# Performance work log

Measured on AMD Instinct MI355X. Metric: run time of the kernel, lower is better.

The kernel has to match this reference:

```python
import jax, jax.numpy as jnp
import numpy as np

B = 1024      # number of states
NP = 32       # SVGD particles per state
AD = 20       # act_dim
OD = 64       # obs_dim
H = 256       # critic hidden width
STEPS = 5     # num_svgd_steps
LR = 0.1      # svgd_lr (adaptive_lr disabled)
SP0 = 1.0     # svgd_sigma_p0
ALIM = 1.0    # act_limit


def _q(obs, X, w1, b1, w2, b2, w3, b3):
    h = jnp.concatenate([obs, X], axis=-1)
    h = jax.nn.relu(h @ w1 + b1)
    h = jax.nn.relu(h @ w2 + b2)
    return jnp.squeeze(h @ w3 + b3, -1)


def _rbf(X):
    # X: [B, NP, AD] -> K [B,NP,NP], diff [B,NP,NP,AD], gamma [B,1,1], K_grad [B,NP,NP,AD]
    diff = X[:, :, None, :] - X[:, None, :, :]
    dist_sq = jnp.sum(diff * diff, axis=-1)
    # adaptive bandwidth via median heuristic (adaptive_sig=True)
    med = jnp.median(dist_sq.reshape(dist_sq.shape[0], -1), axis=-1)
    sig_sq = med / (2.0 * jnp.log(NP + 1.0))
    gamma = (1.0 / (2.0 * sig_sq + 1e-8))[:, None, None]
    K = jnp.exp(-gamma * dist_sq)
    K_grad = -2.0 * gamma[..., None] * diff * K[..., None]  # d/dx_i K(x_i, x_j)
    return K, diff, gamma, K_grad


def setup_inputs():
    key = jax.random.key(0)
    ks = jax.random.split(key, 16)
    N = B * NP

    def lin(k, fi, fo):
        return (jax.random.normal(k, (fi, fo), jnp.float32) / np.sqrt(fi)).astype(jnp.float32)

    return {
        "obs": jax.random.normal(ks[0], (N, OD), jnp.float32),
        "a0": jax.random.normal(ks[1], (N, AD), jnp.float32) * np.sqrt(SP0),
        "q1_w1": lin(ks[2], OD + AD, H), "q1_b1": jnp.zeros((H,), jnp.float32),
        "q1_w2": lin(ks[3], H, H),       "q1_b2": jnp.zeros((H,), jnp.float32),
        "q1_w3": lin(ks[4], H, 1),       "q1_b3": jnp.zeros((1,), jnp.float32),
        "q2_w1": lin(ks[5], OD + AD, H), "q2_b1": jnp.zeros((H,), jnp.float32),
        "q2_w2": lin(ks[6], H, H),       "q2_b2": jnp.zeros((H,), jnp.float32),
        "q2_w3": lin(ks[7], H, 1),       "q2_b3": jnp.zeros((1,), jnp.float32),
    }


def reference(obs, a0, q1_w1, q1_b1, q1_w2, q1_b2, q1_w3, q1_b3,
              q2_w1, q2_b1, q2_w2, q2_b2, q2_w3, q2_b3):
    eye = jnp.eye(NP, dtype=a0.dtype)

    def q_min_sum(Xf):
        q1 = _q(obs, Xf, q1_w1, q1_b1, q1_w2, q1_b2, q1_w3, q1_b3)
        q2 = _q(obs, Xf, q2_w1, q2_b1, q2_w2, q2_b2, q2_w3, q2_b3)
        return jnp.sum(jnp.minimum(q1, q2))

    score_fn = jax.grad(q_min_sum)  # autograd score function

    def step(carry, _):
        a, logp = carry
        score = score_fn(a).reshape(-1, NP, AD)                 # [B,NP,AD]
        X = a.reshape(-1, NP, AD)
        K, diff, gamma, Kg = _rbf(X)
        phi = (jnp.einsum('bij,bjd->bid', K, score) + Kg.sum(axis=1)) / NP
        # log-prob correction terms (with_logprob=True)
        term1 = jnp.mean(jnp.sum(Kg * score[:, None, :, :], axis=-1), axis=2)     # [B,NP]
        inner = jnp.sum(jnp.transpose(Kg, (0, 2, 1, 3)) * diff, axis=-1) \
                - AD * (K - eye)
        term2 = -2.0 * gamma[:, :, 0] * jnp.mean(inner, axis=1)                   # [B,NP]
        logp = logp - LR * (term1 + term2)
        a = a + LR * phi.reshape(a.shape)                        # svgd_optim
        return (a, logp), None

    logp0 = jnp.zeros((B, NP), a0.dtype)
    (a, logp_svgd), _ = jax.lax.scan(step, (a0, logp0), None, length=STEPS)

    a_sq = ALIM * jnp.tanh(a)                                    # [B*NP, AD]
    logp_normal = (-AD * 0.5 * jnp.log(2.0 * jnp.pi * SP0)
                   - 0.5 / SP0 * jnp.sum(a0 * a0, axis=-1)).reshape(-1, NP)
    logp_tanh = -jnp.sum(2.0 * (jnp.log(2.0) - a - jax.nn.softplus(-2.0 * a)),
                         axis=-1).reshape(-1, NP)
    logp_a = jnp.mean(logp_normal + logp_svgd + logp_tanh, axis=-1)  # [B]
    return a_sq, logp_a
```

## Files before the change

kernel.cpp:

```cpp
#include <hip/hip_runtime.h>
#include <math.h>

#define NPART 32
#define ADIM  20
#define ODIM  64
#define HID   256
#define NSTEPS 5
#define LRC   0.1f
#define NBLK  512

typedef short bf8 __attribute__((ext_vector_type(8)));
typedef float f4  __attribute__((ext_vector_type(4)));

#define OW1T(n) ((n)*24576)
#define OW2T(n) (49152 + (n)*65536)
#define OW2C(n) (180224 + (n)*65536)
#define OW1X(n) (311296 + (n)*8192)
#define OW3B(n) (327680 + (n)*256)
#define WS_ELEMS 328192

__device__ __forceinline__ short f2bf(float x) {
    unsigned u = __float_as_uint(x);
    u += 0x7FFFu + ((u >> 16) & 1u);
    return (short)(u >> 16);
}

#define MFMA(a,b,c) __builtin_amdgcn_mfma_f32_16x16x32_bf16((a),(b),(c),0,0,0)

__global__ void prep_weights(const float* __restrict__ w1a, const float* __restrict__ w2a,
                             const float* __restrict__ w3a, const float* __restrict__ w1b,
                             const float* __restrict__ w2b, const float* __restrict__ w3b,
                             unsigned short* __restrict__ ws)
{
    int idx = blockIdx.x * 256 + threadIdx.x;
    if (idx >= WS_ELEMS) return;
    float val;
    if (idx < 49152) {
        int net = idx / 24576, rem = idx % 24576;
        int n = rem / 96, k = rem % 96;
        const float* w1 = net ? w1b : w1a;
        val = (k < 84) ? w1[k*256 + n] : 0.f;
    } else if (idx < 180224) {
        int t2 = idx - 49152; int net = t2 / 65536, rem = t2 % 65536;
        int n = rem / 256, k = rem % 256;
        const float* w2 = net ? w2b : w2a;
        val = w2[k*256 + n];
    } else if (idx < 311296) {
        int t2 = idx - 180224; int net = t2 / 65536, rem = t2 % 65536;
        const float* w2 = net ? w2b : w2a;
        val = w2[rem];
    } else if (idx < 327680) {
        int t2 = idx - 311296; int net = t2 / 8192, rem = t2 % 8192;
        int d = rem / 256, n = rem % 256;
        const float* w1 = net ? w1b : w1a;
        val = (d < 20) ? w1[(64 + d)*256 + n] : 0.f;
    } else {
        int t2 = idx - 327680; int net = t2 / 256, k = t2 % 256;
        const float* w3 = net ? w3b : w3a;
        val = w3[k];
    }
    ws[idx] = (unsigned short)f2bf(val);
}

__global__ void __launch_bounds__(512, 4)
svgd_main(const float* __restrict__ obs,  const float* __restrict__ a0g,
          const float* __restrict__ b1a,  const float* __restrict__ b2a, const float* __restrict__ b3a,
          const float* __restrict__ b1b,  const float* __restrict__ b2b, const float* __restrict__ b3b,
          const float* __restrict__ w3af, const float* __restrict__ w3bf,
          const unsigned short* __restrict__ ws, float* __restrict__ out)
{
    __shared__ __align__(16) short A0s[64*96];
    __shared__ __align__(16) short hbuf[64*264];
    __shared__ unsigned maskS[2][2][64][8];
    __shared__ float Xm[64*20];
    __shared__ float scoreS[64*21];
    __shared__ float phis[64*20];
    __shared__ float qpart[2][8][64];
    __shared__ int   winsS[64];
    __shared__ float logps[64];
    __shared__ unsigned short lutI[496], lutJ[496];
    __shared__ float med2[4];
    __shared__ float qvS[64];

    const int t = threadIdx.x, b = blockIdx.x;
    const int lane = t & 63, wv = t >> 6;
    const int q = lane >> 4, mp = lane & 15;
    const int nb = wv * 32;

    for (int p = t; p < 64*ODIM; p += 512) {
        int i = p >> 6, d = p & 63;
        A0s[i*96 + d] = f2bf(obs[(b*64 + i)*ODIM + d]);
    }
    for (int p = t; p < 64*ADIM; p += 512) {
        int i = p / 20, d = p - i*20;
        float v = a0g[(b*64 + i)*20 + d];
        Xm[p] = v;
        A0s[i*96 + 64 + d] = f2bf(v);
    }
    for (int p = t; p < 64*12; p += 512) { int i = p/12, d = p - i*12; A0s[i*96 + 84 + d] = 0; }
    if (t < 496) {
        int i_ = 0, rem = t;
        while (rem >= 31 - i_) { rem -= 31 - i_; ++i_; }
        lutI[t] = (unsigned short)i_; lutJ[t] = (unsigned short)(i_ + 1 + rem);
    }
    if (t < 64) logps[t] = 0.f;
    __syncthreads();

    for (int step = 0; step < NSTEPS; ++step) {
        { unsigned* mz = &maskS[0][0][0][0];
          for (int p = t; p < 2*2*64*8; p += 512) mz[p] = 0u; }
        __syncthreads();

        for (int net = 0; net < 2; ++net) {
            const unsigned short* w1t = ws + OW1T(net);
            const unsigned short* w2t = ws + OW2T(net);
            const float* b1p = net ? b1b : b1a;
            const float* b2p = net ? b2b : b2a;
            const float* w3p = net ? w3bf : w3af;

            f4 acc[4][2];
            #pragma unroll
            for (int h = 0; h < 4; ++h) { acc[h][0] = (f4){0,0,0,0}; acc[h][1] = (f4){0,0,0,0}; }
            {
                const unsigned short* bp0 = w1t + (size_t)(nb +      mp)*96 + q*8;
                const unsigned short* bp1 = w1t + (size_t)(nb + 16 + mp)*96 + q*8;
                bf8 bb0 = *(const bf8*)bp0, bb1 = *(const bf8*)bp1;
                #pragma unroll
                for (int k0 = 0; k0 < 96; k0 += 32) {
                    bf8 n0 = bb0, n1 = bb1;
                    if (k0 + 32 < 96) { n0 = *(const bf8*)(bp0 + k0 + 32); n1 = *(const bf8*)(bp1 + k0 + 32); }
                    #pragma unroll
                    for (int h = 0; h < 4; ++h) {
                        bf8 aa = *(const bf8*)&A0s[(h*16 + mp)*96 + k0 + q*8];
                        acc[h][0] = MFMA(aa, bb0, acc[h][0]);
                        acc[h][1] = MFMA(aa, bb1, acc[h][1]);
                    }
                    bb0 = n0; bb1 = n1;
                }
            }
            #pragma unroll
            for (int h = 0; h < 4; ++h) {
                #pragma unroll
                for (int s = 0; s < 2; ++s) {
                    int n0 = nb + s*16, col = n0 + mp;
                    float bias = b1p[col];
                    #pragma unroll
                    for (int r = 0; r < 4; ++r) {
                        float v = acc[h][s][r] + bias;
                        bool pos = v > 0.f;
                        unsigned long long bal = __ballot(pos);
                        hbuf[(h*16 + q*4 + r)*264 + col] = f2bf(pos ? v : 0.f);
                        if (mp == 0)
                            atomicOr(&maskS[net][0][h*16 + q*4 + r][n0 >> 5],
                                     ((unsigned)((bal >> (q*16)) & 0xFFFFull)) << (n0 & 16));
                    }
                }
            }
            __syncthreads();

            #pragma unroll
            for (int h = 0; h < 4; ++h) { acc[h][0] = (f4){0,0,0,0}; acc[h][1] = (f4){0,0,0,0}; }
            {
                const unsigned short* bp0 = w2t + (size_t)(nb +      mp)*256 + q*8;
                const unsigned short* bp1 = w2t + (size_t)(nb + 16 + mp)*256 + q*8;
                bf8 bb0 = *(const bf8*)bp0, bb1 = *(const bf8*)bp1;
                #pragma unroll
                for (int k0 = 0; k0 < 256; k0 += 32) {
                    bf8 n0 = bb0, n1 = bb1;
                    if (k0 + 32 < 256) { n0 = *(const bf8*)(bp0 + k0 + 32); n1 = *(const bf8*)(bp1 + k0 + 32); }
                    #pragma unroll
                    for (int h = 0; h < 4; ++h) {
                        bf8 aa = *(const bf8*)&hbuf[(h*16 + mp)*264 + k0 + q*8];
                        acc[h][0] = MFMA(aa, bb0, acc[h][0]);
                        acc[h][1] = MFMA(aa, bb1, acc[h][1]);
                    }
                    bb0 = n0; bb1 = n1;
                }
            }
            {
                float qp[4][4] = {{0,0,0,0},{0,0,0,0},{0,0,0,0},{0,0,0,0}};
                #pragma unroll
                for (int h = 0; h < 4; ++h) {
                    #pragma unroll
                    for (int s = 0; s < 2; ++s) {
                        int n0 = nb + s*16, col = n0 + mp;
                        float bias = b2p[col], w3v = w3p[col];
                        #pragma unroll
                        for (int r = 0; r < 4; ++r) {
                            float v = acc[h][s][r] + bias;
                            bool pos = v > 0.f;
                            unsigned long long bal = __ballot(pos);
                            if (mp == 0)
                                atomicOr(&maskS[net][1][h*16 + q*4 + r][n0 >> 5],
                                         ((unsigned)((bal >> (q*16)) & 0xFFFFull)) << (n0 & 16));
                            qp[h][r] += pos ? v * w3v : 0.f;
                        }
                    }
                }
                #pragma unroll
                for (int d = 1; d < 16; d <<= 1)
                    #pragma unroll
                    for (int h = 0; h < 4; ++h)
                        #pragma unroll
                        for (int r = 0; r < 4; ++r)
                            qp[h][r] += __shfl_xor(qp[h][r], d, 64);
                if (mp == 0) {
                    #pragma unroll
                    for (int h = 0; h < 4; ++h)
                        #pragma unroll
                        for (int r = 0; r < 4; ++r)
                            qpart[net][wv][h*16 + q*4 + r] = qp[h][r];
                }
            }
            __syncthreads();
        }

        if (t < 64) {
            float q0 = b3a[0], q1 = b3b[0];
            #pragma unroll
            for (int w = 0; w < 8; ++w) { q0 += qpart[0][w][t]; q1 += qpart[1][w][t]; }
            winsS[t] = (q0 <= q1) ? 0 : 1;
        }
        __syncthreads();

        for (int net = 0; net < 2; ++net) {
            const unsigned short* w2c  = ws + OW2C(net);
            const unsigned short* w3b8 = ws + OW3B(net);

            f4 acc[4][2];
            #pragma unroll
            for (int h = 0; h < 4; ++h) { acc[h][0] = (f4){0,0,0,0}; acc[h][1] = (f4){0,0,0,0}; }
            int win[4];
            #pragma unroll
            for (int h = 0; h < 4; ++h) win[h] = (winsS[h*16 + mp] == net);
            {
                const unsigned short* bp0 = w2c + (size_t)(nb +      mp)*256 + q*8;
                const unsigned short* bp1 = w2c + (size_t)(nb + 16 + mp)*256 + q*8;
                bf8 bb0 = *(const bf8*)bp0, bb1 = *(const bf8*)bp1;
                #pragma unroll
                for (int k0 = 0; k0 < 256; k0 += 32) {
                    bf8 n0 = bb0, n1 = bb1;
                    if (k0 + 32 < 256) { n0 = *(const bf8*)(bp0 + k0 + 32); n1 = *(const bf8*)(bp1 + k0 + 32); }
                    bf8 w3v = *(const bf8*)(w3b8 + k0 + q*8);
                    #pragma unroll
                    for (int h = 0; h < 4; ++h) {
                        unsigned bits = win[h] ? ((maskS[net][1][h*16 + mp][k0 >> 5] >> (q*8)) & 0xFFu) : 0u;
                        bf8 aa;
                        #pragma unroll
                        for (int j = 0; j < 8; ++j)
                            aa[j] = ((bits >> j) & 1u) ? w3v[j] : (short)0;
                        acc[h][0] = MFMA(aa, bb0, acc[h][0]);
                        acc[h][1] = MFMA(aa, bb1, acc[h][1]);
                    }
                    bb0 = n0; bb1 = n1;
                }
            }
            #pragma unroll
            for (int h = 0; h < 4; ++h) {
                #pragma unroll
                for (int s = 0; s < 2; ++s) {
                    int col = nb + s*16 + mp;
                    #pragma unroll
                    for (int r = 0; r < 4; ++r) {
                        int row = h*16 + q*4 + r;
                        bool on = (maskS[net][0][row][col >> 5] >> (col & 31)) & 1u;
                        hbuf[row*264 + col] = f2bf(on ? acc[h][s][r] : 0.f);
                    }
                }
            }
            __syncthreads();
            {
                int mt = wv & 3, ch = wv >> 2;
                const unsigned short* w1x = ws + OW1X(net);
                const unsigned short* bp  = w1x + (size_t)(ch*16 + mp)*256 + q*8;
                f4 sa = (f4){0,0,0,0};
                bf8 bx = *(const bf8*)bp;
                #pragma unroll
                for (int k0 = 0; k0 < 256; k0 += 32) {
                    bf8 nx = bx;
                    if (k0 + 32 < 256) nx = *(const bf8*)(bp + k0 + 32);
                    bf8 aa = *(const bf8*)&hbuf[(mt*16 + mp)*264 + k0 + q*8];
                    sa = MFMA(aa, bx, sa);
                    bx = nx;
                }
                int colD = ch*16 + mp;
                if (colD < 20) {
                    #pragma unroll
                    for (int r = 0; r < 4; ++r) {
                        int row = mt*16 + q*4 + r;
                        if (net == 0) scoreS[row*21 + colD]  = sa[r];
                        else          scoreS[row*21 + colD] += sa[r];
                    }
                }
            }
            __syncthreads();
        }

        float* d2s   = (float*)hbuf;
        float* dots  = d2s + 2048;
        float* Kms   = dots + 2048;
        float* Spair = Kms + 2048;
        for (int p = t; p < 2048; p += 512) {
            int st = p >> 10, i = (p >> 5) & 31, j = p & 31;
            float s = 0.f;
            #pragma unroll
            for (int d = 0; d < 20; ++d) {
                float df = Xm[(st*32 + i)*20 + d] - Xm[(st*32 + j)*20 + d];
                s += df * df;
            }
            d2s[p] = s;
        }
        __syncthreads();
        if (wv < 2) {
            const float* base = d2s + wv*1024;
            float v[8];
            #pragma unroll
            for (int i = 0; i < 8; ++i) {
                int e = lane*8 + i;
                v[i] = (e < 496) ? base[lutI[e]*32 + lutJ[e]] : 3.4e38f;
            }
            for (int k = 2; k <= 512; k <<= 1) {
                for (int jj = k >> 1; jj >= 8; jj >>= 1) {
                    int lm = jj >> 3;
                    #pragma unroll
                    for (int i = 0; i < 8; ++i) {
                        float w = __shfl_xor(v[i], lm, 64);
                        int p = lane*8 + i;
                        bool takeMin = (((p & k) == 0) == ((p & jj) == 0));
                        v[i] = takeMin ? fminf(v[i], w) : fmaxf(v[i], w);
                    }
                }
                int jj0 = (k >> 1) < 4 ? (k >> 1) : 4;
                for (int jj = jj0; jj >= 1; jj >>= 1) {
                    #pragma unroll
                    for (int i = 0; i < 8; ++i) {
                        if ((i & jj) == 0) {
                            int i2 = i | jj;
                            int p = lane*8 + i;
                            bool up = ((p & k) == 0);
                            float x = v[i], y = v[i2];
                            float mn = fminf(x, y), mx = fmaxf(x, y);
                            v[i] = up ? mn : mx; v[i2] = up ? mx : mn;
                        }
                    }
                }
            }
            if (lane == 29) med2[wv*2 + 0] = v[7];
            if (lane == 30) med2[wv*2 + 1] = v[0];
        } else {
            for (int p = t - 128; p < 2048; p += 384) {
                int st = p >> 10, i = (p >> 5) & 31, j = p & 31;
                float s = 0.f;
                #pragma unroll
                for (int d = 0; d < 20; ++d)
                    s += (Xm[(st*32 + i)*20 + d] - Xm[(st*32 + j)*20 + d])
                         * scoreS[(st*32 + j)*21 + d];
                dots[p] = s;
            }
        }
        __syncthreads();
        for (int p = t; p < 2048; p += 512) {
            int st = p >> 10, i = (p >> 5) & 31, j = p & 31;
            float med   = 0.5f * (med2[st*2] + med2[st*2 + 1]);
            float gamma = 1.f / (2.f * (med / (2.f * logf(33.f))) + 1e-8f);
            float Kij = expf(-gamma * d2s[p]);
            Kms[p] = Kij;
            float c1  = -2.f * gamma * Kij * dots[p];
            float inn = 2.f * gamma * Kij * d2s[p] - 20.f * (Kij - (i == j ? 1.f : 0.f));
            Spair[st*1056 + i*33 + j] = c1 - 2.f * gamma * inn;
        }
        __syncthreads();
        {
            int i = t & 63, dg = t >> 6;
            int st = i >> 5, il = i & 31;
            float med   = 0.5f * (med2[st*2] + med2[st*2 + 1]);
            float gamma = 1.f / (2.f * (med / (2.f * logf(33.f))) + 1e-8f);
            for (int dd = dg; dd < 20; dd += 8) {
                float xi = Xm[i*20 + dd];
                float s = 0.f;
                for (int j = 0; j < 32; ++j) {
                    float Kij = Kms[st*1024 + il*32 + j];
                    s += Kij * (scoreS[(st*32 + j)*21 + dd]
                                + 2.f * gamma * (xi - Xm[(st*32 + j)*20 + dd]));
                }
                phis[i*20 + dd] = s * (1.f/32.f);
            }
        }
        if (t < 64) {
            int st = t >> 5;
            float s = 0.f;
            #pragma unroll
            for (int j = 0; j < 32; ++j) s += Spair[st*1056 + (t & 31)*33 + j];
            logps[t] -= LRC * (s * (1.f/32.f));
        }
        __syncthreads();
        for (int p = t; p < 64*20; p += 512) {
            int i = p / 20, d = p - i*20;
            float nx = Xm[p] + LRC * phis[p];
            Xm[p] = nx;
            A0s[i*96 + 64 + d] = f2bf(nx);
        }
        __syncthreads();
    }

    for (int p = t; p < 64*20; p += 512) {
        int i = p / 20, d = p - i*20;
        out[(b*64 + i)*20 + d] = tanhf(Xm[p]);
    }
    if (t < 64) {
        float lt = 0.f, s0 = 0.f;
        for (int d = 0; d < 20; ++d) {
            float a  = Xm[t*20 + d];
            float x  = -2.f * a;
            float sp = fmaxf(x, 0.f) + log1pf(expf(-fabsf(x)));
            lt -= 2.f * (0.69314718056f - a - sp);
            float v = a0g[(b*64 + t)*20 + d];
            s0 += v * v;
        }
        qvS[t] = -18.3787706641f - 0.5f*s0 + logps[t] + lt;
    }
    __syncthreads();
    if (t < 2) {
        float s = 0.f;
        for (int i = 0; i < 32; ++i) s += qvS[t*32 + i];
        out[1024*32*20 + b*2 + t] = s * (1.f/32.f);
    }
}

extern "C" void kernel_launch(void* const* d_in, const int* in_sizes, int n_in,
                              void* d_out, int out_size, void* d_ws, size_t ws_size,
                              hipStream_t stream) {
    unsigned short* ws = (unsigned short*)d_ws;
    prep_weights<<<(WS_ELEMS + 255)/256, 256, 0, stream>>>(
        (const float*)d_in[2],  (const float*)d_in[4],  (const float*)d_in[6],
        (const float*)d_in[8],  (const float*)d_in[10], (const float*)d_in[12], ws);
    svgd_main<<<NBLK, 512, 0, stream>>>(
        (const float*)d_in[0],  (const float*)d_in[1],
        (const float*)d_in[3],  (const float*)d_in[5],  (const float*)d_in[7],
        (const float*)d_in[9],  (const float*)d_in[11], (const float*)d_in[13],
        (const float*)d_in[6],  (const float*)d_in[12],
        ws, (float*)d_out);
}
```

Before: 500.1 us.

## Compute SVGD kernel terms via bf16 MFMA Gram matrices and fused row reductions

Pairwise squared distances and score dot products become bf16 MFMA Gram products (norms plus cross terms), and the K·score and K·X sums that give phi also run on MFMA. The log-prob correction is folded into per-row shuffle reductions instead of a full pairwise Spair matrix, and mask clearing is overlapped with the median sort. The float-to-bf16 conversion switches from round-to-nearest to truncation. Together these cut LDS traffic, scalar FLOPs and barriers in the per-step SVGD update, at the cost of accuracy loss from bf16 and norm-expansion cancellation in the distances.

```diff
diff --git a/kernel.cpp b/kernel.cpp
--- a/kernel.cpp
+++ b/kernel.cpp
@@ -8,6 +8,7 @@
 #define NSTEPS 5
 #define LRC   0.1f
 #define NBLK  512
+#define LOG33 3.4965075614664802f
 
 typedef short bf8 __attribute__((ext_vector_type(8)));
 typedef float f4  __attribute__((ext_vector_type(4)));
@@ -23,6 +24,12 @@
     unsigned u = __float_as_uint(x);
     u += 0x7FFFu + ((u >> 16) & 1u);
     return (short)(u >> 16);
+}
+__device__ __forceinline__ short f2bfT(float x) {
+    return (short)(__float_as_uint(x) >> 16);
+}
+__device__ __forceinline__ float bf2f(short s) {
+    return __uint_as_float(((unsigned)(unsigned short)s) << 16);
 }
 
 #define MFMA(a,b,c) __builtin_amdgcn_mfma_f32_16x16x32_bf16((a),(b),(c),0,0,0)
@@ -74,13 +81,20 @@
     __shared__ unsigned maskS[2][2][64][8];
     __shared__ float Xm[64*20];
     __shared__ float scoreS[64*21];
-    __shared__ float phis[64*20];
     __shared__ float qpart[2][8][64];
     __shared__ int   winsS[64];
     __shared__ float logps[64];
     __shared__ unsigned short lutI[496], lutJ[496];
     __shared__ float med2[4];
     __shared__ float qvS[64];
+    __shared__ float normsS[64], diagS[64], rowKS[64];
+
+    float* d2sF = (float*)hbuf;
+    float* GSF  = ((float*)hbuf) + 2048;
+    short* KbS  = hbuf + 8192;
+    short* SBs  = hbuf + 10240;
+    short* STbS = hbuf + 12288;
+    short* XTbS = hbuf + 14336;
 
     const int t = threadIdx.x, b = blockIdx.x;
     const int lane = t & 63, wv = t >> 6;
@@ -89,15 +103,17 @@
 
     for (int p = t; p < 64*ODIM; p += 512) {
         int i = p >> 6, d = p & 63;
-        A0s[i*96 + d] = f2bf(obs[(b*64 + i)*ODIM + d]);
+        A0s[i*96 + d] = f2bfT(obs[(b*64 + i)*ODIM + d]);
     }
     for (int p = t; p < 64*ADIM; p += 512) {
         int i = p / 20, d = p - i*20;
         float v = a0g[(b*64 + i)*20 + d];
         Xm[p] = v;
-        A0s[i*96 + 64 + d] = f2bf(v);
+        A0s[i*96 + 64 + d] = f2bfT(v);
     }
     for (int p = t; p < 64*12; p += 512) { int i = p/12, d = p - i*12; A0s[i*96 + 84 + d] = 0; }
+    { unsigned* mz = &maskS[0][0][0][0];
+      for (int p = t; p < 2*2*64*8; p += 512) mz[p] = 0u; }
     if (t < 496) {
         int i_ = 0, rem = t;
         while (rem >= 31 - i_) { rem -= 31 - i_; ++i_; }
@@ -107,10 +123,6 @@
     __syncthreads();
 
     for (int step = 0; step < NSTEPS; ++step) {
-        { unsigned* mz = &maskS[0][0][0][0];
-          for (int p = t; p < 2*2*64*8; p += 512) mz[p] = 0u; }
-        __syncthreads();
-
         for (int net = 0; net < 2; ++net) {
             const unsigned short* w1t = ws + OW1T(net);
             const unsigned short* w2t = ws + OW2T(net);
@@ -149,7 +161,7 @@
                         float v = acc[h][s][r] + bias;
                         bool pos = v > 0.f;
                         unsigned long long bal = __ballot(pos);
-                        hbuf[(h*16 + q*4 + r)*264 + col] = f2bf(pos ? v : 0.f);
+                        hbuf[(h*16 + q*4 + r)*264 + col] = f2bfT(pos ? v : 0.f);
                         if (mp == 0)
                             atomicOr(&maskS[net][0][h*16 + q*4 + r][n0 >> 5],
                                      ((unsigned)((bal >> (q*16)) & 0xFFFFull)) << (n0 & 16));
@@ -264,7 +276,7 @@
                     for (int r = 0; r < 4; ++r) {
                         int row = h*16 + q*4 + r;
                         bool on = (maskS[net][0][row][col >> 5] >> (col & 31)) & 1u;
-                        hbuf[row*264 + col] = f2bf(on ? acc[h][s][r] : 0.f);
+                        hbuf[row*264 + col] = f2bfT(on ? acc[h][s][r] : 0.f);
                     }
                 }
             }
@@ -296,23 +308,48 @@
             __syncthreads();
         }
 
-        float* d2s   = (float*)hbuf;
-        float* dots  = d2s + 2048;
-        float* Kms   = dots + 2048;
-        float* Spair = Kms + 2048;
-        for (int p = t; p < 2048; p += 512) {
-            int st = p >> 10, i = (p >> 5) & 31, j = p & 31;
-            float s = 0.f;
+        if (t < 64) {
+            int st = t >> 5;
+            float nrm = 0.f, dg = 0.f;
             #pragma unroll
             for (int d = 0; d < 20; ++d) {
-                float df = Xm[(st*32 + i)*20 + d] - Xm[(st*32 + j)*20 + d];
-                s += df * df;
-            }
-            d2s[p] = s;
-        }
-        __syncthreads();
+                float xb = bf2f(A0s[t*96 + 64 + d]);
+                nrm += xb * xb;
+                float sv = scoreS[t*21 + d];
+                float xv = Xm[t*20 + d];
+                dg += xv * sv;
+                short sb = f2bfT(sv);
+                SBs[t*32 + d] = sb;
+                STbS[st*1024 + d*32 + (t & 31)] = sb;
+                XTbS[st*1024 + d*32 + (t & 31)] = f2bfT(xv);
+            }
+            #pragma unroll
+            for (int d = 20; d < 32; ++d) SBs[t*32 + d] = 0;
+            normsS[t] = nrm;
+            diagS[t]  = dg;
+        }
+        __syncthreads();
+
+        {
+            int stw = wv >> 2, mt = (wv >> 1) & 1, nt = wv & 1;
+            bf8 aa  = *(const bf8*)&A0s[(stw*32 + mt*16 + mp)*96 + 64 + q*8];
+            bf8 bbx = *(const bf8*)&A0s[(stw*32 + nt*16 + mp)*96 + 64 + q*8];
+            bf8 bbs = *(const bf8*)&SBs[(stw*32 + nt*16 + mp)*32 + q*8];
+            f4 gx = MFMA(aa, bbx, ((f4){0,0,0,0}));
+            f4 gs = MFMA(aa, bbs, ((f4){0,0,0,0}));
+            int jl = nt*16 + mp;
+            float nj = normsS[stw*32 + jl];
+            #pragma unroll
+            for (int r = 0; r < 4; ++r) {
+                int il = mt*16 + q*4 + r;
+                d2sF[stw*1024 + il*32 + jl] = normsS[stw*32 + il] + nj - 2.f*gx[r];
+                GSF [stw*1024 + il*32 + jl] = gs[r];
+            }
+        }
+        __syncthreads();
+
         if (wv < 2) {
-            const float* base = d2s + wv*1024;
+            const float* base = d2sF + wv*1024;
             float v[8];
             #pragma unroll
             for (int i = 0; i < 8; ++i) {
@@ -348,57 +385,65 @@
             if (lane == 29) med2[wv*2 + 0] = v[7];
             if (lane == 30) med2[wv*2 + 1] = v[0];
         } else {
-            for (int p = t - 128; p < 2048; p += 384) {
-                int st = p >> 10, i = (p >> 5) & 31, j = p & 31;
-                float s = 0.f;
-                #pragma unroll
-                for (int d = 0; d < 20; ++d)
-                    s += (Xm[(st*32 + i)*20 + d] - Xm[(st*32 + j)*20 + d])
-                         * scoreS[(st*32 + j)*21 + d];
-                dots[p] = s;
-            }
-        }
-        __syncthreads();
-        for (int p = t; p < 2048; p += 512) {
-            int st = p >> 10, i = (p >> 5) & 31, j = p & 31;
-            float med   = 0.5f * (med2[st*2] + med2[st*2 + 1]);
-            float gamma = 1.f / (2.f * (med / (2.f * logf(33.f))) + 1e-8f);
-            float Kij = expf(-gamma * d2s[p]);
-            Kms[p] = Kij;
-            float c1  = -2.f * gamma * Kij * dots[p];
-            float inn = 2.f * gamma * Kij * d2s[p] - 20.f * (Kij - (i == j ? 1.f : 0.f));
-            Spair[st*1056 + i*33 + j] = c1 - 2.f * gamma * inn;
-        }
-        __syncthreads();
+            unsigned* mz = &maskS[0][0][0][0];
+            for (int p = t - 128; p < 2*2*64*8; p += 384) mz[p] = 0u;
+        }
+        __syncthreads();
+
         {
-            int i = t & 63, dg = t >> 6;
-            int st = i >> 5, il = i & 31;
-            float med   = 0.5f * (med2[st*2] + med2[st*2 + 1]);
-            float gamma = 1.f / (2.f * (med / (2.f * logf(33.f))) + 1e-8f);
-            for (int dd = dg; dd < 20; dd += 8) {
-                float xi = Xm[i*20 + dd];
-                float s = 0.f;
-                for (int j = 0; j < 32; ++j) {
-                    float Kij = Kms[st*1024 + il*32 + j];
-                    s += Kij * (scoreS[(st*32 + j)*21 + dd]
-                                + 2.f * gamma * (xi - Xm[(st*32 + j)*20 + dd]));
-                }
-                phis[i*20 + dd] = s * (1.f/32.f);
-            }
-        }
-        if (t < 64) {
-            int st = t >> 5;
-            float s = 0.f;
-            #pragma unroll
-            for (int j = 0; j < 32; ++j) s += Spair[st*1056 + (t & 31)*33 + j];
-            logps[t] -= LRC * (s * (1.f/32.f));
-        }
-        __syncthreads();
-        for (int p = t; p < 64*20; p += 512) {
-            int i = p / 20, d = p - i*20;
-            float nx = Xm[p] + LRC * phis[p];
-            Xm[p] = nx;
-            A0s[i*96 + 64 + d] = f2bf(nx);
+            int i = t >> 3, stw = i >> 5, il = i & 31, j0 = (t & 7) * 4;
+            float medv = 0.5f * (med2[stw*2] + med2[stw*2 + 1]);
+            float gam  = 1.f / (2.f * (medv / (2.f * LOG33)) + 1e-8f);
+            float sK = 0.f, sKGS = 0.f, sKd2 = 0.f, sKdg = 0.f;
+            #pragma unroll
+            for (int jj = 0; jj < 4; ++jj) {
+                int j = j0 + jj;
+                float d2 = d2sF[stw*1024 + il*32 + j];
+                float K  = expf(-gam * d2);
+                KbS[stw*1024 + il*32 + j] = f2bfT(K);
+                sK   += K;
+                sKGS += K * GSF[stw*1024 + il*32 + j];
+                sKd2 += K * d2;
+                sKdg += K * diagS[stw*32 + j];
+            }
+            #pragma unroll
+            for (int d = 1; d < 8; d <<= 1) {
+                sK   += __shfl_xor(sK,   d, 64);
+                sKGS += __shfl_xor(sKGS, d, 64);
+                sKd2 += __shfl_xor(sKd2, d, 64);
+                sKdg += __shfl_xor(sKdg, d, 64);
+            }
+            if ((t & 7) == 0) {
+                rowKS[i] = sK;
+                float sdots = sKGS - sKdg;
+                float ssum  = -2.f*gam*sdots
+                              - 2.f*gam*(2.f*gam*sKd2 - 20.f*(sK - 1.f));
+                logps[i] -= LRC * (ssum * (1.f/32.f));
+            }
+        }
+        __syncthreads();
+
+        {
+            int stw = wv >> 2, mt = (wv >> 1) & 1, nt = wv & 1;
+            float medv = 0.5f * (med2[stw*2] + med2[stw*2 + 1]);
+            float gam  = 1.f / (2.f * (medv / (2.f * LOG33)) + 1e-8f);
+            bf8 aa  = *(const bf8*)&KbS [stw*1024 + (mt*16 + mp)*32 + q*8];
+            bf8 b1v = *(const bf8*)&STbS[stw*1024 + (nt*16 + mp)*32 + q*8];
+            bf8 b2v = *(const bf8*)&XTbS[stw*1024 + (nt*16 + mp)*32 + q*8];
+            f4 ks = MFMA(aa, b1v, ((f4){0,0,0,0}));
+            f4 kx = MFMA(aa, b2v, ((f4){0,0,0,0}));
+            int dd = nt*16 + mp;
+            if (dd < 20) {
+                #pragma unroll
+                for (int r = 0; r < 4; ++r) {
+                    int gi = stw*32 + mt*16 + q*4 + r;
+                    float xi  = Xm[gi*20 + dd];
+                    float phi = (ks[r] + 2.f*gam*(xi*rowKS[gi] - kx[r])) * (1.f/32.f);
+                    float nx  = xi + LRC * phi;
+                    Xm[gi*20 + dd] = nx;
+                    A0s[gi*96 + 64 + dd] = f2bfT(nx);
+                }
+            }
         }
         __syncthreads();
     }
```

Measured after the change: 497.5 us. About the same (-0.5%).
